# Kernel tuning notes

Measured on AMD Instinct MI355X. Metric: run time of the kernel, lower is better.

## Reference

```python
import jax, jax.numpy as jnp
import numpy as np


def setup_inputs() -> dict:
    key = jax.random.key(0)
    k1, k2 = jax.random.split(key)
    B, D, H, W = 16, 64, 64, 64
    K = 1024  # codebook_size
    x = jax.random.normal(k1, (B, D, H, W), dtype=jnp.float32)
    codebook = jax.random.normal(k2, (K, D), dtype=jnp.float32)
    return {"x": x, "codebook": codebook}


def reference(x, codebook):
    """VQ quantization: nearest-codebook lookup.

    x: (B, D, H, W) latent features; codebook: (K, D).
    Returns (quantized (B, D, H, W), indices (B, H, W)).
    """
    B, D, H, W = x.shape
    # (B, D, H, W) -> (B*H*W, D)
    flat = jnp.transpose(x, (0, 2, 3, 1)).reshape(-1, D)
    d2 = (
        jnp.sum(flat * flat, axis=-1, keepdims=True)
        - 2.0 * (flat @ codebook.T)
        + jnp.sum(codebook * codebook, axis=-1)
    )
    idx = jnp.argmin(d2, axis=-1)  # (N,)
    quantized = codebook[idx]  # (N, D) gather
    quantized = quantized.reshape(B, H, W, D).transpose(0, 3, 1, 2)
    return quantized, idx.reshape(B, H, W)
```

## Files before the change

kernel.cpp:

```cpp
#include <hip/hip_runtime.h>
#include <hip/hip_bf16.h>

#define D_ 64
#define HW_ 4096
#define K_ 1024
#define NPTS_ 65536
#define QOUT_ 4194304
#define DELTA 0.006f
#define INF_ 3.4e38f

typedef short bf16x8 __attribute__((ext_vector_type(8)));
typedef float f32x4 __attribute__((ext_vector_type(4)));

__device__ __forceinline__ void gload_lds16(const float* g, float* l) {
    __builtin_amdgcn_global_load_lds((const __attribute__((address_space(1))) void*)g,
                                     (__attribute__((address_space(3))) void*)l, 16, 0, 0);
}
__device__ __forceinline__ void gload_lds4(const float* g, float* l) {
    __builtin_amdgcn_global_load_lds((const __attribute__((address_space(1))) void*)g,
                                     (__attribute__((address_space(3))) void*)l, 4, 0, 0);
}

__global__ __launch_bounds__(256) void vq_pack(const float* __restrict__ cb,
                                               float* __restrict__ cnorm,
                                               short* __restrict__ P) {
    const int t = blockIdx.x * 256 + threadIdx.x;
    const int gch = t >> 6, l = t & 63;
    const int j  = gch * 16 + (l & 15);
    const int dg = l >> 4;
#pragma unroll
    for (int s = 0; s < 2; ++s) {
        const float* src = cb + j * D_ + s * 32 + dg * 8;
        short hb[8], lb[8];
#pragma unroll
        for (int i = 0; i < 8; ++i) {
            const float v = -2.f * src[i];
            __hip_bfloat16 h = __float2bfloat16(v);
            hb[i] = *(const short*)&h;
            const float r = v - __bfloat162float(h);
            __hip_bfloat16 lo = __float2bfloat16(r);
            lb[i] = *(const short*)&lo;
        }
        short* dh = P + ((size_t)((gch * 2 + s) * 2 + 0) * 64 + l) * 8;
        short* dl = P + ((size_t)((gch * 2 + s) * 2 + 1) * 64 + l) * 8;
#pragma unroll
        for (int i = 0; i < 8; ++i) { dh[i] = hb[i]; dl[i] = lb[i]; }
    }
    if (t < K_) {
        const float4* r = (const float4*)(cb + (size_t)t * D_);
        float s0 = 0.f, s1 = 0.f, s2 = 0.f, s3 = 0.f;
#pragma unroll
        for (int i = 0; i < 16; ++i) {
            float4 v = r[i];
            s0 = fmaf(v.x, v.x, s0); s1 = fmaf(v.y, v.y, s1);
            s2 = fmaf(v.z, v.z, s2); s3 = fmaf(v.w, v.w, s3);
        }
        cnorm[t] = (s0 + s1) + (s2 + s3);
    }
}

__global__ __launch_bounds__(256, 4) void vq_main(const float* __restrict__ x,
                                                  const float* __restrict__ cnorm_g,
                                                  const short* __restrict__ P,
                                                  float* __restrict__ out) {
    __shared__ short cbuf[2][4096];
    __shared__ float cnt[K_];

    const int tid  = threadIdx.x;
    const int lane = tid & 63;
    const int wid  = tid >> 6;
    const int pg   = blockIdx.x;
    const int bb   = pg >> 6;
    const int hw0  = (pg & 63) << 6;

    const float* Pf = (const float*)P;

#pragma unroll
    for (int i = 0; i < 4; ++i)
        gload_lds4(cnorm_g + i * 256 + wid * 64 + lane, cnt + i * 256 + wid * 64);
#pragma unroll
    for (int r = 0; r < 2; ++r)
        gload_lds16(Pf + r * 1024 + wid * 256 + lane * 4,
                    (float*)cbuf[0] + r * 1024 + wid * 256);

    bf16x8 ah[2], al[2];
    {
        const float* xb = x + (size_t)bb * (D_ * HW_) + hw0;
        const int p_l = wid * 16 + (lane & 15);
#pragma unroll
        for (int s = 0; s < 2; ++s) {
            const int d0 = s * 32 + (lane >> 4) * 8;
#pragma unroll
            for (int i = 0; i < 8; ++i) {
                const float v = xb[(size_t)(d0 + i) * HW_ + p_l];
                __hip_bfloat16 h = __float2bfloat16(v);
                ah[s][i] = *(const short*)&h;
                const float r = v - __bfloat162float(h);
                __hip_bfloat16 lo = __float2bfloat16(r);
                al[s][i] = *(const short*)&lo;
            }
        }
    }
    asm volatile("s_waitcnt vmcnt(0)" ::: "memory");
    __syncthreads();

    float m1[4], m2[4];
    int   i1[4];
#pragma unroll
    for (int q = 0; q < 4; ++q) { m1[q] = INF_; m2[q] = INF_; i1[q] = 0; }

    int cur = 0;
#pragma unroll 1
    for (int c = 0; c < 32; ++c) {
        if (c + 1 < 32) {
            const float* src = Pf + (size_t)(c + 1) * 2048;
            float* dst = (float*)cbuf[cur ^ 1];
#pragma unroll
            for (int r = 0; r < 2; ++r)
                gload_lds16(src + r * 1024 + wid * 256 + lane * 4,
                            dst + r * 1024 + wid * 256);
        }
        const bf16x8* fr = (const bf16x8*)cbuf[cur];
#pragma unroll
        for (int u = 0; u < 2; ++u) {
            const int kc = c * 32 + u * 16 + (lane & 15);
            const float cn = cnt[kc];
            bf16x8 bh0 = fr[(u * 4 + 0) * 64 + lane];
            bf16x8 bl0 = fr[(u * 4 + 1) * 64 + lane];
            bf16x8 bh1 = fr[(u * 4 + 2) * 64 + lane];
            bf16x8 bl1 = fr[(u * 4 + 3) * 64 + lane];
            f32x4 aa = {0.f, 0.f, 0.f, 0.f};
            f32x4 ab = {0.f, 0.f, 0.f, 0.f};
            aa = __builtin_amdgcn_mfma_f32_16x16x32_bf16(ah[0], bh0, aa, 0, 0, 0);
            ab = __builtin_amdgcn_mfma_f32_16x16x32_bf16(ah[1], bh1, ab, 0, 0, 0);
            aa = __builtin_amdgcn_mfma_f32_16x16x32_bf16(al[0], bh0, aa, 0, 0, 0);
            ab = __builtin_amdgcn_mfma_f32_16x16x32_bf16(al[1], bh1, ab, 0, 0, 0);
            aa = __builtin_amdgcn_mfma_f32_16x16x32_bf16(ah[0], bl0, aa, 0, 0, 0);
            ab = __builtin_amdgcn_mfma_f32_16x16x32_bf16(ah[1], bl1, ab, 0, 0, 0);
#pragma unroll
            for (int r = 0; r < 4; ++r) {
                const float d2 = cn + (aa[r] + ab[r]);
                const bool lt = d2 < m1[r];
                m2[r] = fminf(m2[r], fmaxf(m1[r], d2));
                m1[r] = fminf(m1[r], d2);
                i1[r] = lt ? kc : i1[r];
            }
        }
        __syncthreads();
        cur ^= 1;
    }

#pragma unroll
    for (int q = 0; q < 4; ++q) {
        float a1 = m1[q], a2 = m2[q];
        int   ai = i1[q];
#pragma unroll
        for (int m = 1; m < 16; m <<= 1) {
            const float o1 = __shfl_xor(a1, m);
            const int   oi = __shfl_xor(ai, m);
            const float o2 = __shfl_xor(a2, m);
            const float nm2 = fminf(fminf(a2, o2), fmaxf(a1, o1));
            if (o1 < a1 || (o1 == a1 && oi < ai)) { a1 = o1; ai = oi; }
            a2 = nm2;
        }
        if ((lane & 15) == 0) {
            const int pt = wid * 16 + 4 * (lane >> 4) + q;
            const bool amb = (a2 - a1 <= DELTA);
            out[(size_t)QOUT_ + pg * 64 + pt] = amb ? -(float)(ai + 1) : (float)ai;
        }
    }
}

__global__ __launch_bounds__(256) void vq_resolve(const float* __restrict__ x,
                                                  const float* __restrict__ cb,
                                                  const float* __restrict__ cnorm_g,
                                                  float* __restrict__ out) {
    __shared__ float tile[64 * 65];
    __shared__ int res_idx[64];
    __shared__ int flist[64];
    __shared__ int fcnt;

    const int tid  = threadIdx.x;
    const int lane = tid & 63;
    const int wid  = tid >> 6;
    const int qg   = blockIdx.x;
    const int bb   = qg >> 6;
    const int col0 = (qg & 63) << 6;
    const int t64  = tid & 63;

    if (tid == 0) fcnt = 0;
    __syncthreads();

    if (tid < 64) {
        const float v = out[(size_t)QOUT_ + qg * 64 + tid];
        const bool fl = v < 0.f;
        res_idx[tid] = fl ? (int)(-v) - 1 : (int)v;
        if (fl) { const int p = atomicAdd(&fcnt, 1); flist[p] = tid; }
    }
    __syncthreads();

    const int nf = fcnt;
    for (int i = wid; i < nf; i += 4) {
        const int pt = flist[i];
        const float* xr = x + (size_t)bb * (D_ * HW_) + col0 + pt;
        float xv[D_];
#pragma unroll
        for (int d = 0; d < D_; ++d) xv[d] = xr[(size_t)d * HW_];
        float b1 = INF_; int bi = 0;
        for (int c = 0; c < 16; ++c) {
            const int row = lane * 16 + c;
            const float4* cr = (const float4*)(cb + (size_t)row * D_);
            float a0 = 0.f, a1 = 0.f, a2 = 0.f, a3 = 0.f;
#pragma unroll
            for (int g = 0; g < 16; ++g) {
                const float4 cf = cr[g];
                a0 = fmaf(xv[4 * g + 0], cf.x, a0);
                a1 = fmaf(xv[4 * g + 1], cf.y, a1);
                a2 = fmaf(xv[4 * g + 2], cf.z, a2);
                a3 = fmaf(xv[4 * g + 3], cf.w, a3);
            }
            const float dot = (a0 + a1) + (a2 + a3);
            const float d2 = fmaf(-2.f, dot, cnorm_g[row]);
            if (d2 < b1) { b1 = d2; bi = row; }
        }
#pragma unroll
        for (int m = 1; m < 64; m <<= 1) {
            const float o1 = __shfl_xor(b1, m);
            const int   oi = __shfl_xor(bi, m);
            if (o1 < b1 || (o1 == b1 && oi < bi)) { b1 = o1; bi = oi; }
        }
        if (lane == 0) res_idx[pt] = bi;
    }
    __syncthreads();

    if (tid < 64) out[(size_t)QOUT_ + qg * 64 + tid] = (float)res_idx[tid];

#pragma unroll
    for (int pass = 0; pass < 4; ++pass) {
        const int pt = pass * 16 + (tid >> 4);
        const int dq = tid & 15;
        const float4 v = *(const float4*)(cb + (size_t)res_idx[pt] * D_ + dq * 4);
        float* dst = &tile[pt * 65 + dq * 4];
        dst[0] = v.x; dst[1] = v.y; dst[2] = v.z; dst[3] = v.w;
    }
    __syncthreads();

    float* op = out + (size_t)bb * (D_ * HW_) + col0 + t64;
#pragma unroll
    for (int dd = 0; dd < 16; ++dd) {
        const int d = (tid >> 6) * 16 + dd;
        op[(size_t)d * HW_] = tile[t64 * 65 + d];
    }
}

extern "C" void kernel_launch(void* const* d_in, const int* in_sizes, int n_in,
                              void* d_out, int out_size, void* d_ws, size_t ws_size,
                              hipStream_t stream) {
    const float* x  = (const float*)d_in[0];
    const float* cb = (const float*)d_in[1];
    float* out   = (float*)d_out;
    float* cnorm = (float*)d_ws;
    short* P     = (short*)((char*)d_ws + 4096);

    vq_pack<<<16, 256, 0, stream>>>(cb, cnorm, P);
    vq_main<<<NPTS_ / 64, 256, 0, stream>>>(x, cnorm, P, out);
    vq_resolve<<<NPTS_ / 64, 256, 0, stream>>>(x, cb, cnorm, out);
}
```

Before: 76.23 us.

## Split codebook across two wave groups in vq_main and vectorize resolve stores

The main kernel now runs 512 threads per block. Two groups of four waves each scan half of every 64-code chunk, so the loop runs 16 iterations instead of 32 and the per-point top-2 results are merged through shared memory at the end. The goal is more latency hiding and more MFMA parallelism per point group, paid for by doubled LDS for the codebook buffer, an extra barrier and a merge step. Separately, the resolve kernel transposes its gathered tile into a d-major layout so the output is written with float4 stores instead of scalar strided stores.

After: 80.32 us. +5.4%, slower.

```diff
diff --git a/kernel.cpp b/kernel.cpp
--- a/kernel.cpp
+++ b/kernel.cpp
@@ -59,34 +59,37 @@
     }
 }
 
-__global__ __launch_bounds__(256, 4) void vq_main(const float* __restrict__ x,
+__global__ __launch_bounds__(512, 4) void vq_main(const float* __restrict__ x,
                                                   const float* __restrict__ cnorm_g,
                                                   const short* __restrict__ P,
                                                   float* __restrict__ out) {
-    __shared__ short cbuf[2][4096];
+    __shared__ short cbuf[2][8192];
     __shared__ float cnt[K_];
+    __shared__ float gm1[2][64], gm2[2][64];
+    __shared__ int   gi1[2][64];
 
     const int tid  = threadIdx.x;
     const int lane = tid & 63;
     const int wid  = tid >> 6;
+    const int tile = wid & 3;
+    const int kg   = wid >> 2;
     const int pg   = blockIdx.x;
     const int bb   = pg >> 6;
     const int hw0  = (pg & 63) << 6;
 
     const float* Pf = (const float*)P;
 
-#pragma unroll
-    for (int i = 0; i < 4; ++i)
-        gload_lds4(cnorm_g + i * 256 + wid * 64 + lane, cnt + i * 256 + wid * 64);
+    gload_lds4(cnorm_g + wid * 64 + lane, cnt + wid * 64);
+    gload_lds4(cnorm_g + 512 + wid * 64 + lane, cnt + 512 + wid * 64);
 #pragma unroll
     for (int r = 0; r < 2; ++r)
-        gload_lds16(Pf + r * 1024 + wid * 256 + lane * 4,
-                    (float*)cbuf[0] + r * 1024 + wid * 256);
+        gload_lds16(Pf + r * 2048 + wid * 256 + lane * 4,
+                    (float*)cbuf[0] + r * 2048 + wid * 256);
 
     bf16x8 ah[2], al[2];
     {
         const float* xb = x + (size_t)bb * (D_ * HW_) + hw0;
-        const int p_l = wid * 16 + (lane & 15);
+        const int p_l = tile * 16 + (lane & 15);
 #pragma unroll
         for (int s = 0; s < 2; ++s) {
             const int d0 = s * 32 + (lane >> 4) * 8;
@@ -111,24 +114,25 @@
 
     int cur = 0;
 #pragma unroll 1
-    for (int c = 0; c < 32; ++c) {
-        if (c + 1 < 32) {
-            const float* src = Pf + (size_t)(c + 1) * 2048;
+    for (int c = 0; c < 16; ++c) {
+        if (c + 1 < 16) {
+            const float* src = Pf + (size_t)(c + 1) * 4096;
             float* dst = (float*)cbuf[cur ^ 1];
 #pragma unroll
             for (int r = 0; r < 2; ++r)
-                gload_lds16(src + r * 1024 + wid * 256 + lane * 4,
-                            dst + r * 1024 + wid * 256);
+                gload_lds16(src + r * 2048 + wid * 256 + lane * 4,
+                            dst + r * 2048 + wid * 256);
         }
         const bf16x8* fr = (const bf16x8*)cbuf[cur];
 #pragma unroll
         for (int u = 0; u < 2; ++u) {
-            const int kc = c * 32 + u * 16 + (lane & 15);
+            const int gl = kg * 2 + u;
+            const int kc = c * 64 + gl * 16 + (lane & 15);
             const float cn = cnt[kc];
-            bf16x8 bh0 = fr[(u * 4 + 0) * 64 + lane];
-            bf16x8 bl0 = fr[(u * 4 + 1) * 64 + lane];
-            bf16x8 bh1 = fr[(u * 4 + 2) * 64 + lane];
-            bf16x8 bl1 = fr[(u * 4 + 3) * 64 + lane];
+            bf16x8 bh0 = fr[(gl * 4 + 0) * 64 + lane];
+            bf16x8 bl0 = fr[(gl * 4 + 1) * 64 + lane];
+            bf16x8 bh1 = fr[(gl * 4 + 2) * 64 + lane];
+            bf16x8 bl1 = fr[(gl * 4 + 3) * 64 + lane];
             f32x4 aa = {0.f, 0.f, 0.f, 0.f};
             f32x4 ab = {0.f, 0.f, 0.f, 0.f};
             aa = __builtin_amdgcn_mfma_f32_16x16x32_bf16(ah[0], bh0, aa, 0, 0, 0);
@@ -164,10 +168,22 @@
             a2 = nm2;
         }
         if ((lane & 15) == 0) {
-            const int pt = wid * 16 + 4 * (lane >> 4) + q;
-            const bool amb = (a2 - a1 <= DELTA);
-            out[(size_t)QOUT_ + pg * 64 + pt] = amb ? -(float)(ai + 1) : (float)ai;
-        }
+            const int pt = tile * 16 + 4 * (lane >> 4) + q;
+            gm1[kg][pt] = a1; gm2[kg][pt] = a2; gi1[kg][pt] = ai;
+        }
+    }
+    __syncthreads();
+
+    if (tid < 64) {
+        const float a1 = gm1[0][tid], a2 = gm2[0][tid];
+        const int   ai = gi1[0][tid];
+        const float b1 = gm1[1][tid], b2 = gm2[1][tid];
+        const int   bi = gi1[1][tid];
+        float f1, f2; int fi;
+        if (b1 < a1 || (b1 == a1 && bi < ai)) { f1 = b1; fi = bi; f2 = fminf(b2, a1); }
+        else                                  { f1 = a1; fi = ai; f2 = fminf(a2, b1); }
+        const bool amb = (f2 - f1 <= DELTA);
+        out[(size_t)QOUT_ + pg * 64 + tid] = amb ? -(float)(fi + 1) : (float)fi;
     }
 }
 
@@ -175,7 +191,7 @@
                                                   const float* __restrict__ cb,
                                                   const float* __restrict__ cnorm_g,
                                                   float* __restrict__ out) {
-    __shared__ float tile[64 * 65];
+    __shared__ float tile[64 * 68];
     __shared__ int res_idx[64];
     __shared__ int flist[64];
     __shared__ int fcnt;
@@ -186,7 +202,6 @@
     const int qg   = blockIdx.x;
     const int bb   = qg >> 6;
     const int col0 = (qg & 63) << 6;
-    const int t64  = tid & 63;
 
     if (tid == 0) fcnt = 0;
     __syncthreads();
@@ -240,16 +255,20 @@
         const int pt = pass * 16 + (tid >> 4);
         const int dq = tid & 15;
         const float4 v = *(const float4*)(cb + (size_t)res_idx[pt] * D_ + dq * 4);
-        float* dst = &tile[pt * 65 + dq * 4];
-        dst[0] = v.x; dst[1] = v.y; dst[2] = v.z; dst[3] = v.w;
-    }
-    __syncthreads();
-
-    float* op = out + (size_t)bb * (D_ * HW_) + col0 + t64;
-#pragma unroll
-    for (int dd = 0; dd < 16; ++dd) {
-        const int d = (tid >> 6) * 16 + dd;
-        op[(size_t)d * HW_] = tile[t64 * 65 + d];
+        tile[(dq * 4 + 0) * 68 + pt] = v.x;
+        tile[(dq * 4 + 1) * 68 + pt] = v.y;
+        tile[(dq * 4 + 2) * 68 + pt] = v.z;
+        tile[(dq * 4 + 3) * 68 + pt] = v.w;
+    }
+    __syncthreads();
+
+    float* ob = out + (size_t)bb * (D_ * HW_) + col0;
+#pragma unroll
+    for (int i = 0; i < 4; ++i) {
+        const int g = tid & 15;
+        const int d = (tid >> 4) + i * 16;
+        const float4 q = *(const float4*)&tile[d * 68 + g * 4];
+        *(float4*)(ob + (size_t)d * HW_ + g * 4) = q;
     }
 }
 
@@ -263,6 +282,6 @@
     short* P     = (short*)((char*)d_ws + 4096);
 
     vq_pack<<<16, 256, 0, stream>>>(cb, cnorm, P);
-    vq_main<<<NPTS_ / 64, 256, 0, stream>>>(x, cnorm, P, out);
+    vq_main<<<NPTS_ / 64, 512, 0, stream>>>(x, cnorm, P, out);
     vq_resolve<<<NPTS_ / 64, 256, 0, stream>>>(x, cb, cnorm, out);
 }
```
